# Kernel tuning notes

Hardware: AMD Instinct MI355X
Metric: run time of the kernel (lower is better)

## Reference

```python
import jax, jax.numpy as jnp
import numpy as np

B, S, D = 2, 2048, 1024
H, DK = 16, 64


def setup_inputs() -> dict:
    key = jax.random.key(0)
    ks = jax.random.split(key, 10)
    scale = D ** -0.5
    x = jax.random.normal(ks[0], (B, S, D), dtype=jnp.float32)
    mask = jax.random.randint(ks[1], (B, S), 0, 2) > 0  # True = masked positions
    Wq = jax.random.normal(ks[2], (D, H * DK), dtype=jnp.float32) * scale
    Wk = jax.random.normal(ks[3], (D, H * DK), dtype=jnp.float32) * scale
    Wv = jax.random.normal(ks[4], (D, H * DK), dtype=jnp.float32) * scale
    Wo = jax.random.normal(ks[5], (H * DK, D), dtype=jnp.float32) * scale
    bq = jnp.zeros((H * DK,), jnp.float32)
    bk = jnp.zeros((H * DK,), jnp.float32)
    bv = jnp.zeros((H * DK,), jnp.float32)
    bo = jnp.zeros((D,), jnp.float32)
    return {"x": x, "mask": mask, "Wq": Wq, "bq": bq, "Wk": Wk, "bk": bk,
            "Wv": Wv, "bv": bv, "Wo": Wo, "bo": bo}


def reference(x, mask, Wq, bq, Wk, bk, Wv, bv, Wo, bo):
    b, s, _ = x.shape
    # Linear + activation (dropout is identity at eval)
    q = jax.nn.relu(x @ Wq + bq).reshape(b, s, H, DK)
    k = jax.nn.relu(x @ Wk + bk).reshape(b, s, H, DK)
    v = jax.nn.relu(x @ Wv + bv).reshape(b, s, H, DK)
    # scores: [B, H, Sq, Sk]
    attn = jnp.einsum("bqhd,bkhd->bhqk", q, k) * (DK ** -0.5)
    # NOTE: original uses masked_fill(mask, 1e-9) BEFORE softmax (not -inf)
    attn = jnp.where(mask[:, None, None, :], jnp.float32(1e-9), attn)
    attn = jax.nn.softmax(attn, axis=-1)
    out = jnp.einsum("bhqk,bkhd->bqhd", attn, v).reshape(b, s, H * DK)
    return jax.nn.relu(out @ Wo + bo)
```

## Files before the change

### kernel.cpp

```cpp
#include <hip/hip_runtime.h>
#include <stdint.h>

typedef __attribute__((ext_vector_type(8))) short short8;
typedef __attribute__((ext_vector_type(4))) short short4b;
typedef __attribute__((ext_vector_type(4))) float f32x4;
typedef __attribute__((ext_vector_type(4))) unsigned short ushort4_t;

#define MFMA16(a, b, c) __builtin_amdgcn_mfma_f32_16x16x32_bf16((a), (b), (c), 0, 0, 0)

#if defined(__HIP_DEVICE_COMPILE__)
  #if __has_builtin(__builtin_amdgcn_mfma_f32_16x16x16bf16_1k)
    #define MFMA16K16(a, b, c) __builtin_amdgcn_mfma_f32_16x16x16bf16_1k((a), (b), (c), 0, 0, 0)
  #else
    #define MFMA16K16(a, b, c) __builtin_amdgcn_mfma_f32_16x16x16_bf16((a), (b), (c), 0, 0, 0)
  #endif
#else
  #define MFMA16K16(a, b, c) (c)
#endif

#define SCL_F (0.125f * 1.44269504f)

__device__ __forceinline__ float b2f(unsigned short u) {
    union { unsigned u; float f; } c; c.u = ((unsigned)u) << 16; return c.f;
}
__device__ __forceinline__ unsigned short f2b(float f) {
    union { float f; unsigned u; } c; c.f = f;
    unsigned r = c.u + 0x7FFF + ((c.u >> 16) & 1);
    return (unsigned short)(r >> 16);
}
__device__ __forceinline__ unsigned f_as_u(float f) {
    union { float f; unsigned u; } c; c.f = f; return c.u;
}

__device__ __forceinline__ void g2lds16(const unsigned short* g, unsigned lds_byte_off) {
    __builtin_amdgcn_global_load_lds(
        (const __attribute__((address_space(1))) void*)(uintptr_t)g,
        (__attribute__((address_space(3))) void*)(uintptr_t)lds_byte_off,
        16, 0, 0);
}

__global__ void detect_dtype(const unsigned short* __restrict__ x, int* __restrict__ flag) {
    __shared__ int cnt;
    if (threadIdx.x == 0) cnt = 0;
    __syncthreads();
    int insane = 0;
    #pragma unroll
    for (int j = 0; j < 4; ++j) {
        unsigned short u = x[threadIdx.x * 4 + j];
        int e = (u >> 7) & 0xFF;
        if ((e >= 1 && e <= 90) || e >= 165) insane++;
    }
    atomicAdd(&cnt, insane);
    __syncthreads();
    if (threadIdx.x == 0) *flag = (cnt > 128) ? 1 : 0;
}

__global__ __launch_bounds__(256) void convtrans_k(const void* __restrict__ s0, const void* __restrict__ s1,
                                                   const void* __restrict__ s2, const void* __restrict__ s3,
                                                   const void* __restrict__ b0, const void* __restrict__ b1,
                                                   const void* __restrict__ b2, const void* __restrict__ b3s,
                                                   const void* __restrict__ xsrc,
                                                   unsigned short* __restrict__ xdst,
                                                   unsigned short* __restrict__ dstBase,
                                                   unsigned short* __restrict__ dstB3,
                                                   unsigned short* __restrict__ dstBo,
                                                   const int* __restrict__ flag) {
    const int z = blockIdx.z;
    if (z >= 5) {
        if (!*flag) return;
        const int slice = z - 5;
        const size_t i0 = (size_t)slice * 524288 + (blockIdx.y * 16 + blockIdx.x) * 2048 + threadIdx.x * 8;
        const float* s = (const float*)xsrc;
        float4 f0 = *(const float4*)&s[i0];
        float4 f1 = *(const float4*)&s[i0 + 4];
        unsigned short* t = &xdst[i0];
        t[0] = f2b(f0.x); t[1] = f2b(f0.y); t[2] = f2b(f0.z); t[3] = f2b(f0.w);
        t[4] = f2b(f1.x); t[5] = f2b(f1.y); t[6] = f2b(f1.z); t[7] = f2b(f1.w);
        return;
    }
    if (z == 4) {
        if (blockIdx.y != 0 || blockIdx.x >= 4) return;
        const int w = blockIdx.x;
        const void* src = (w == 0) ? b0 : (w == 1) ? b1 : (w == 2) ? b2 : b3s;
        const float bscl = (w == 0) ? SCL_F : 1.0f;
        #pragma unroll
        for (int j = 0; j < 4; ++j) {
            const int i = threadIdx.x * 4 + j;
            float fv = (*flag) ? ((const float*)src)[i] : b2f(((const unsigned short*)src)[i]);
            unsigned short v = f2b(fv * bscl);
            if (w < 3) dstB3[w * 1024 + i] = v;
            else dstBo[i] = v;
        }
        return;
    }
    __shared__ __align__(16) unsigned short tile[64 * 72];
    const void* src = (z == 0) ? s0 : (z == 1) ? s1 : (z == 2) ? s2 : s3;
    unsigned short* dst = dstBase + (size_t)z * 1024 * 1024;
    const float wscl = (z == 0) ? SCL_F : 1.0f;
    const int tid = threadIdx.x;
    const int r0 = blockIdx.y * 64, c0 = blockIdx.x * 64;
    const int rb = tid >> 3, c = (tid & 7) * 8;
    if (*flag) {
        const float* s = (const float*)src;
        #pragma unroll
        for (int it = 0; it < 2; ++it) {
            int rr = it * 32 + rb;
            float4 f0 = *(const float4*)&s[(size_t)(r0 + rr) * 1024 + c0 + c];
            float4 f1 = *(const float4*)&s[(size_t)(r0 + rr) * 1024 + c0 + c + 4];
            unsigned short* t = &tile[rr * 72 + c];
            t[0] = f2b(f0.x * wscl); t[1] = f2b(f0.y * wscl); t[2] = f2b(f0.z * wscl); t[3] = f2b(f0.w * wscl);
            t[4] = f2b(f1.x * wscl); t[5] = f2b(f1.y * wscl); t[6] = f2b(f1.z * wscl); t[7] = f2b(f1.w * wscl);
        }
    } else if (z == 0) {
        const unsigned short* s = (const unsigned short*)src;
        #pragma unroll
        for (int it = 0; it < 2; ++it) {
            int rr = it * 32 + rb;
            union { short8 v; unsigned short u[8]; } in;
            in.v = *(const short8*)&s[(size_t)(r0 + rr) * 1024 + c0 + c];
            unsigned short* t = &tile[rr * 72 + c];
            #pragma unroll
            for (int j = 0; j < 8; ++j) t[j] = f2b(b2f(in.u[j]) * SCL_F);
        }
    } else {
        const unsigned short* s = (const unsigned short*)src;
        #pragma unroll
        for (int it = 0; it < 2; ++it) {
            int rr = it * 32 + rb;
            *(short8*)&tile[rr * 72 + c] = *(const short8*)&s[(size_t)(r0 + rr) * 1024 + c0 + c];
        }
    }
    __syncthreads();
    #pragma unroll
    for (int it = 0; it < 2; ++it) {
        int n = it * 32 + rb, k8 = c;
        union { short8 s; unsigned short u[8]; } tmp;
        #pragma unroll
        for (int j = 0; j < 8; ++j) tmp.u[j] = tile[(k8 + j) * 72 + n];
        *(short8*)&dst[(size_t)(c0 + n) * 1024 + r0 + k8] = tmp.s;
    }
}

__global__ __launch_bounds__(256) void mask_k(unsigned short* __restrict__ qkv,
                                              const int* __restrict__ mask) {
    const int row = blockIdx.x * 2 + (threadIdx.x >> 7);
    const int col = (threadIdx.x & 127) * 8;
    if (mask[row]) {
        const short8 z = {0, 0, 0, 0, 0, 0, 0, 0};
        *(short8*)&qkv[(size_t)row * 3072 + 1024 + col] = z;
    }
}

__global__ __launch_bounds__(256) void gemm_bias_relu(const unsigned short* __restrict__ A,
                                                      const void* __restrict__ Araw,
                                                      const unsigned short* __restrict__ BT,
                                                      const unsigned short* __restrict__ bias,
                                                      void* __restrict__ C,
                                                      unsigned short* __restrict__ VtG,
                                                      const int* __restrict__ flag,
                                                      int M, int N, int K, int mode) {
    __shared__ __align__(16) unsigned short As[128 * 32];
    __shared__ __align__(16) unsigned short Bs[128 * 32];
    const int tid = threadIdx.x;
    const int wave = tid >> 6, lane = tid & 63;
    const int quad = lane >> 4, l16 = lane & 15;
    const int wm = wave >> 1, wn = wave & 1;
    const int m0 = blockIdx.y * 128, n0 = blockIdx.x * 128;

    const unsigned short* Ause = (Araw != nullptr && *flag == 0) ? (const unsigned short*)Araw : A;

    f32x4 acc[4][4];
    #pragma unroll
    for (int i = 0; i < 4; i++)
        #pragma unroll
        for (int j = 0; j < 4; j++) acc[i][j] = (f32x4){0.f, 0.f, 0.f, 0.f};

    const int srow = wave * 32 + (lane >> 2);
    const int sc8  = (lane & 3) * 8;
    const unsigned short* gA0 = Ause + (size_t)(m0 + srow) * K + sc8;
    const unsigned short* gA1 = gA0 + (size_t)16 * K;
    const unsigned short* gB0 = BT + (size_t)(n0 + srow) * K + sc8;
    const unsigned short* gB1 = gB0 + (size_t)16 * K;
    const unsigned ldsA = (unsigned)(uintptr_t)&As[0] + wave * 2048;
    const unsigned ldsB = (unsigned)(uintptr_t)&Bs[0] + wave * 2048;

    for (int k0 = 0; k0 < K; k0 += 32) {
        __syncthreads();
        g2lds16(gA0 + k0, ldsA);
        g2lds16(gA1 + k0, ldsA + 1024);
        g2lds16(gB0 + k0, ldsB);
        g2lds16(gB1 + k0, ldsB + 1024);
        __syncthreads();
        short8 af[4], bf[4];
        #pragma unroll
        for (int i = 0; i < 4; i++) af[i] = *(const short8*)&As[(wm * 64 + i * 16 + l16) * 32 + quad * 8];
        #pragma unroll
        for (int j = 0; j < 4; j++) bf[j] = *(const short8*)&Bs[(wn * 64 + j * 16 + l16) * 32 + quad * 8];
        #pragma unroll
        for (int i = 0; i < 4; i++)
            #pragma unroll
            for (int j = 0; j < 4; j++)
                acc[i][j] = MFMA16(af[i], bf[j], acc[i][j]);
    }

    if (mode == 2 && n0 >= 2048) {
        #pragma unroll
        for (int j = 0; j < 4; j++) {
            const int col = n0 + wn * 64 + j * 16 + l16;
            const int h  = (col - 2048) >> 6;
            const int dk = (col - 2048) & 63;
            const float bj = b2f(bias[col]);
            #pragma unroll
            for (int i = 0; i < 4; i++) {
                const int rowb = m0 + wm * 64 + i * 16 + quad * 4;
                const int bb = rowb >> 11;
                const int s0 = rowb & 2047;
                ushort4_t w;
                #pragma unroll
                for (int r = 0; r < 4; r++) {
                    float v = acc[i][j][r] + bj;
                    v = v > 0.f ? v : 0.f;
                    w[r] = f2b(v);
                }
                *(ushort4_t*)&VtG[(size_t)((bb * 16 + h) * 64 + dk) * 2048 + s0] = w;
            }
        }
    } else {
        const int f32out = (mode == 1) && (*flag != 0);
        #pragma unroll
        for (int j = 0; j < 4; j++) {
            const int col = n0 + wn * 64 + j * 16 + l16;
            const float bj = b2f(bias[col]);
            #pragma unroll
            for (int i = 0; i < 4; i++) {
                const int rowb = m0 + wm * 64 + i * 16 + quad * 4;
                #pragma unroll
                for (int r = 0; r < 4; r++) {
                    float v = acc[i][j][r] + bj;
                    v = v > 0.f ? v : 0.f;
                    if (f32out) ((float*)C)[(size_t)(rowb + r) * N + col] = v;
                    else ((unsigned short*)C)[(size_t)(rowb + r) * N + col] = f2b(v);
                }
            }
        }
    }
}

__global__ __launch_bounds__(256) void attn_kernel(const unsigned short* __restrict__ qkv,
                                                   const unsigned short* __restrict__ VtG,
                                                   unsigned short* __restrict__ out) {
    __shared__ __align__(16) unsigned short Ks[64 * 72];
    __shared__ __align__(16) unsigned short Vs[64 * 72];

    const int qt = blockIdx.x, bh = blockIdx.y;
    const int b = bh >> 4, h = bh & 15;
    const int tid = threadIdx.x, wave = tid >> 6, lane = tid & 63;
    const int quad = lane >> 4, l16 = lane & 15;

    const int qrowA = qt * 128 + wave * 16 + l16;
    const unsigned short* qpA = qkv + (size_t)(b * 2048 + qrowA) * 3072 + h * 64;
    const unsigned short* qpB = qpA + (size_t)64 * 3072;
    const short8 qa0 = *(const short8*)(qpA + quad * 8);
    const short8 qa1 = *(const short8*)(qpA + 32 + quad * 8);
    const short8 qb0 = *(const short8*)(qpB + quad * 8);
    const short8 qb1 = *(const short8*)(qpB + 32 + quad * 8);

    f32x4 oA[4], oB[4], sumA, sumB;
    #pragma unroll
    for (int n = 0; n < 4; n++) { oA[n] = (f32x4){0.f,0.f,0.f,0.f}; oB[n] = (f32x4){0.f,0.f,0.f,0.f}; }
    sumA = (f32x4){0.f,0.f,0.f,0.f};
    sumB = (f32x4){0.f,0.f,0.f,0.f};

    const short4b ones = { (short)0x3F80, (short)0x3F80, (short)0x3F80, (short)0x3F80 };

    const int srow = tid >> 2;
    const int scol = (tid & 3) * 16;
    const unsigned short* kg = qkv + (size_t)(b * 2048 + srow) * 3072 + 1024 + h * 64 + scol;
    const unsigned short* vg = VtG + (size_t)(bh * 64 + srow) * 2048 + scol;
    const size_t kstep = (size_t)64 * 3072;
    unsigned short* wK = &Ks[srow * 72 + scol];
    unsigned short* wV = &Vs[srow * 72 + scol];

    for (int kt = 0; kt < 32; ++kt) {
        __syncthreads();
        *(short8*)wK       = *(const short8*)(kg + kt * kstep);
        *(short8*)(wK + 8) = *(const short8*)(kg + kt * kstep + 8);
        *(short8*)wV       = *(const short8*)(vg + kt * 64);
        *(short8*)(wV + 8) = *(const short8*)(vg + kt * 64 + 8);
        __syncthreads();

        f32x4 sA[4], sB[4];
        #pragma unroll
        for (int t = 0; t < 4; ++t) {
            const short8 kb0 = *(const short8*)&Ks[(t * 16 + l16) * 72 + quad * 8];
            const short8 kb1 = *(const short8*)&Ks[(t * 16 + l16) * 72 + 32 + quad * 8];
            f32x4 z = (f32x4){0.f, 0.f, 0.f, 0.f};
            sA[t] = MFMA16(kb1, qa1, MFMA16(kb0, qa0, z));
            sB[t] = MFMA16(kb1, qb1, MFMA16(kb0, qb0, z));
        }

        short4b vb[4][4];
        #pragma unroll
        for (int t = 0; t < 4; ++t)
            #pragma unroll
            for (int n = 0; n < 4; ++n)
                vb[t][n] = *(const short4b*)&Vs[(n * 16 + l16) * 72 + t * 16 + quad * 4];

        #pragma unroll
        for (int t = 0; t < 4; ++t) {
            float pA[4], pB[4];
            #pragma unroll
            for (int r = 0; r < 4; ++r) {
                pA[r] = exp2f(sA[t][r]);
                pB[r] = exp2f(sB[t][r]);
            }
            union { unsigned u[2]; short4b s; } fa, fb;
            fa.u[0] = __builtin_amdgcn_perm(f_as_u(pA[1]), f_as_u(pA[0]), 0x07060302u);
            fa.u[1] = __builtin_amdgcn_perm(f_as_u(pA[3]), f_as_u(pA[2]), 0x07060302u);
            fb.u[0] = __builtin_amdgcn_perm(f_as_u(pB[1]), f_as_u(pB[0]), 0x07060302u);
            fb.u[1] = __builtin_amdgcn_perm(f_as_u(pB[3]), f_as_u(pB[2]), 0x07060302u);
            #pragma unroll
            for (int n = 0; n < 4; ++n) {
                oA[n] = MFMA16K16(fa.s, vb[t][n], oA[n]);
                oB[n] = MFMA16K16(fb.s, vb[t][n], oB[n]);
            }
            sumA = MFMA16K16(fa.s, ones, sumA);
            sumB = MFMA16K16(fb.s, ones, sumB);
        }
    }

    float invA[4], invB[4];
    #pragma unroll
    for (int r = 0; r < 4; ++r) { invA[r] = 1.0f / sumA[r]; invB[r] = 1.0f / sumB[r]; }
    #pragma unroll
    for (int n = 0; n < 4; n++)
        #pragma unroll
        for (int r = 0; r < 4; r++) {
            const int row = qt * 128 + wave * 16 + quad * 4 + r;
            out[(size_t)(b * 2048 + row) * 1024 + h * 64 + n * 16 + l16] = f2b(oA[n][r] * invA[r]);
            out[(size_t)(b * 2048 + row + 64) * 1024 + h * 64 + n * 16 + l16] = f2b(oB[n][r] * invB[r]);
        }
}

extern "C" void kernel_launch(void* const* d_in, const int* in_sizes, int n_in,
                              void* d_out, int out_size, void* d_ws, size_t ws_size,
                              hipStream_t stream) {
    const void* x  = d_in[0];
    const int*  mk = (const int*)d_in[1];
    const void* Wq = d_in[2]; const void* bq = d_in[3];
    const void* Wk = d_in[4]; const void* bk = d_in[5];
    const void* Wv = d_in[6]; const void* bv = d_in[7];
    const void* Wo = d_in[8]; const void* bo = d_in[9];

    char* wsb = (char*)d_ws;
    int* flag = (int*)wsb;
    unsigned short* W0 = (unsigned short*)(wsb + 64);

    const size_t M1 = 1024u * 1024u;
    const size_t M4 = 4096u * 1024u;
    unsigned short* xb  = W0;
    unsigned short* WT  = xb + M4;
    unsigned short* WoT = WT + 3 * M1;
    unsigned short* b3  = WoT + M1;
    unsigned short* bob = b3 + 4096;
    unsigned short* qkv = bob + 1024;
    unsigned short* VtG = qkv + (size_t)4096 * 3072;
    unsigned short* abf = xb;

    detect_dtype<<<1, 256, 0, stream>>>((const unsigned short*)x, flag);

    convtrans_k<<<dim3(16, 16, 13), 256, 0, stream>>>(Wq, Wk, Wv, Wo, bq, bk, bv, bo,
                                                      x, xb, WT, b3, bob, flag);

    gemm_bias_relu<<<dim3(24, 32), 256, 0, stream>>>(xb, x, WT, b3, qkv, VtG, flag,
                                                     4096, 3072, 1024, 2);
    mask_k<<<2048, 256, 0, stream>>>(qkv, mk);
    attn_kernel<<<dim3(16, 32), 256, 0, stream>>>(qkv, VtG, abf);
    gemm_bias_relu<<<dim3(8, 32), 256, 0, stream>>>(abf, nullptr, WoT, bob, d_out, VtG, flag,
                                                    4096, 1024, 1024, 1);
}
```

Before: 235.7 us.

## Prefetch next K/V tile into registers, XOR-swizzle LDS, raise MFMA priority

The attention kernel now loads the next K and V tile from global memory into registers while the current tile is being computed. This hides global-load latency behind the MFMA work. The padded 72-wide LDS rows become 64-wide rows with an XOR swizzle on 8-element groups, which avoids bank conflicts and shrinks shared memory. s_setprio raises wave priority around the compute section. The register prefetch costs extra VGPRs, which may reduce occupancy.

```diff
diff --git a/kernel.cpp b/kernel.cpp
--- a/kernel.cpp
+++ b/kernel.cpp
@@ -249,8 +249,8 @@
 __global__ __launch_bounds__(256) void attn_kernel(const unsigned short* __restrict__ qkv,
                                                    const unsigned short* __restrict__ VtG,
                                                    unsigned short* __restrict__ out) {
-    __shared__ __align__(16) unsigned short Ks[64 * 72];
-    __shared__ __align__(16) unsigned short Vs[64 * 72];
+    __shared__ __align__(16) unsigned short Ks[64 * 64];
+    __shared__ __align__(16) unsigned short Vs[64 * 64];
 
     const int qt = blockIdx.x, bh = blockIdx.y;
     const int b = bh >> 4, h = bh & 15;
@@ -275,25 +275,42 @@
 
     const int srow = tid >> 2;
     const int scol = (tid & 3) * 16;
+    const int sxor = (srow & 7) << 3;
     const unsigned short* kg = qkv + (size_t)(b * 2048 + srow) * 3072 + 1024 + h * 64 + scol;
     const unsigned short* vg = VtG + (size_t)(bh * 64 + srow) * 2048 + scol;
     const size_t kstep = (size_t)64 * 3072;
-    unsigned short* wK = &Ks[srow * 72 + scol];
-    unsigned short* wV = &Vs[srow * 72 + scol];
+    unsigned short* wK0 = &Ks[(srow * 64 + scol) ^ sxor];
+    unsigned short* wK1 = &Ks[(srow * 64 + scol + 8) ^ sxor];
+    unsigned short* wV0 = &Vs[(srow * 64 + scol) ^ sxor];
+    unsigned short* wV1 = &Vs[(srow * 64 + scol + 8) ^ sxor];
+
+    const int rx = (l16 & 7) << 3;
+
+    short8 rk0 = *(const short8*)(kg);
+    short8 rk1 = *(const short8*)(kg + 8);
+    short8 rv0 = *(const short8*)(vg);
+    short8 rv1 = *(const short8*)(vg + 8);
 
     for (int kt = 0; kt < 32; ++kt) {
         __syncthreads();
-        *(short8*)wK       = *(const short8*)(kg + kt * kstep);
-        *(short8*)(wK + 8) = *(const short8*)(kg + kt * kstep + 8);
-        *(short8*)wV       = *(const short8*)(vg + kt * 64);
-        *(short8*)(wV + 8) = *(const short8*)(vg + kt * 64 + 8);
+        *(short8*)wK0 = rk0;
+        *(short8*)wK1 = rk1;
+        *(short8*)wV0 = rv0;
+        *(short8*)wV1 = rv1;
+        if (kt < 31) {
+            rk0 = *(const short8*)(kg + (kt + 1) * kstep);
+            rk1 = *(const short8*)(kg + (kt + 1) * kstep + 8);
+            rv0 = *(const short8*)(vg + (kt + 1) * 64);
+            rv1 = *(const short8*)(vg + (kt + 1) * 64 + 8);
+        }
         __syncthreads();
 
+        __builtin_amdgcn_s_setprio(1);
         f32x4 sA[4], sB[4];
         #pragma unroll
         for (int t = 0; t < 4; ++t) {
-            const short8 kb0 = *(const short8*)&Ks[(t * 16 + l16) * 72 + quad * 8];
-            const short8 kb1 = *(const short8*)&Ks[(t * 16 + l16) * 72 + 32 + quad * 8];
+            const short8 kb0 = *(const short8*)&Ks[(((t * 16 + l16) * 64) + quad * 8) ^ rx];
+            const short8 kb1 = *(const short8*)&Ks[(((t * 16 + l16) * 64) + 32 + quad * 8) ^ rx];
             f32x4 z = (f32x4){0.f, 0.f, 0.f, 0.f};
             sA[t] = MFMA16(kb1, qa1, MFMA16(kb0, qa0, z));
             sB[t] = MFMA16(kb1, qb1, MFMA16(kb0, qb0, z));
@@ -304,7 +321,7 @@
         for (int t = 0; t < 4; ++t)
             #pragma unroll
             for (int n = 0; n < 4; ++n)
-                vb[t][n] = *(const short4b*)&Vs[(n * 16 + l16) * 72 + t * 16 + quad * 4];
+                vb[t][n] = *(const short4b*)&Vs[(((n * 16 + l16) * 64) + t * 16 + quad * 4) ^ rx];
 
         #pragma unroll
         for (int t = 0; t < 4; ++t) {
@@ -327,6 +344,7 @@
             sumA = MFMA16K16(fa.s, ones, sumA);
             sumB = MFMA16K16(fb.s, ones, sumB);
         }
+        __builtin_amdgcn_s_setprio(0);
     }
 
     float invA[4], invB[4];
```

Measured after the change: 227.2 us. -3.6%, faster.

## Pipeline GEMM and attention K/V loads with multi-buffered LDS and swizzle

Applied to the files above, without the earlier changes.

The GEMM now uses a three-stage LDS ring filled by async global-to-LDS loads, gated by vmcnt waits, so loads for later K-steps overlap the current MFMAs. The attention kernel double-buffers K/V tiles through registers, swaps padded LDS rows for an XOR swizzle, and remaps block indices for locality. It also raises wave priority during MFMA work and uses the hardware exp2 builtin. The intent is to hide global-load latency and cut barrier stalls, at the cost of more LDS (possibly lower occupancy) and fragile hand-set wait counts.

```diff
diff --git a/kernel.cpp b/kernel.cpp
--- a/kernel.cpp
+++ b/kernel.cpp
@@ -14,8 +14,14 @@
   #else
     #define MFMA16K16(a, b, c) __builtin_amdgcn_mfma_f32_16x16x16_bf16((a), (b), (c), 0, 0, 0)
   #endif
+  #if __has_builtin(__builtin_amdgcn_exp2f)
+    #define EXP2(x) __builtin_amdgcn_exp2f(x)
+  #else
+    #define EXP2(x) exp2f(x)
+  #endif
 #else
   #define MFMA16K16(a, b, c) (c)
+  #define EXP2(x) exp2f(x)
 #endif
 
 #define SCL_F (0.125f * 1.44269504f)
@@ -159,8 +165,8 @@
                                                       unsigned short* __restrict__ VtG,
                                                       const int* __restrict__ flag,
                                                       int M, int N, int K, int mode) {
-    __shared__ __align__(16) unsigned short As[128 * 32];
-    __shared__ __align__(16) unsigned short Bs[128 * 32];
+    __shared__ __align__(16) unsigned short As[3][128 * 32];
+    __shared__ __align__(16) unsigned short Bs[3][128 * 32];
     const int tid = threadIdx.x;
     const int wave = tid >> 6, lane = tid & 63;
     const int quad = lane >> 4, l16 = lane & 15;
@@ -181,26 +187,60 @@
     const unsigned short* gA1 = gA0 + (size_t)16 * K;
     const unsigned short* gB0 = BT + (size_t)(n0 + srow) * K + sc8;
     const unsigned short* gB1 = gB0 + (size_t)16 * K;
-    const unsigned ldsA = (unsigned)(uintptr_t)&As[0] + wave * 2048;
-    const unsigned ldsB = (unsigned)(uintptr_t)&Bs[0] + wave * 2048;
+
+    unsigned lA0 = (unsigned)(uintptr_t)&As[0][0] + wave * 2048;
+    unsigned lA1 = (unsigned)(uintptr_t)&As[1][0] + wave * 2048;
+    unsigned lA2 = (unsigned)(uintptr_t)&As[2][0] + wave * 2048;
+    unsigned lB0 = (unsigned)(uintptr_t)&Bs[0][0] + wave * 2048;
+    unsigned lB1 = (unsigned)(uintptr_t)&Bs[1][0] + wave * 2048;
+    unsigned lB2 = (unsigned)(uintptr_t)&Bs[2][0] + wave * 2048;
+    const unsigned short* pA0 = &As[0][0];
+    const unsigned short* pA1 = &As[1][0];
+    const unsigned short* pA2 = &As[2][0];
+    const unsigned short* pB0 = &Bs[0][0];
+    const unsigned short* pB1 = &Bs[1][0];
+    const unsigned short* pB2 = &Bs[2][0];
+
+    g2lds16(gA0, lA0); g2lds16(gA1, lA0 + 1024);
+    g2lds16(gB0, lB0); g2lds16(gB1, lB0 + 1024);
+    if (32 < K) {
+        g2lds16(gA0 + 32, lA1); g2lds16(gA1 + 32, lA1 + 1024);
+        g2lds16(gB0 + 32, lB1); g2lds16(gB1 + 32, lB1 + 1024);
+    }
+    if (64 < K) {
+        g2lds16(gA0 + 64, lA2); g2lds16(gA1 + 64, lA2 + 1024);
+        g2lds16(gB0 + 64, lB2); g2lds16(gB1 + 64, lB2 + 1024);
+    }
 
     for (int k0 = 0; k0 < K; k0 += 32) {
-        __syncthreads();
-        g2lds16(gA0 + k0, ldsA);
-        g2lds16(gA1 + k0, ldsA + 1024);
-        g2lds16(gB0 + k0, ldsB);
-        g2lds16(gB1 + k0, ldsB + 1024);
-        __syncthreads();
+        if (k0 + 64 < K)       asm volatile("s_waitcnt vmcnt(8)" ::: "memory");
+        else if (k0 + 32 < K)  asm volatile("s_waitcnt vmcnt(4)" ::: "memory");
+        else                   asm volatile("s_waitcnt vmcnt(0)" ::: "memory");
+        __builtin_amdgcn_s_barrier();
+
         short8 af[4], bf[4];
         #pragma unroll
-        for (int i = 0; i < 4; i++) af[i] = *(const short8*)&As[(wm * 64 + i * 16 + l16) * 32 + quad * 8];
-        #pragma unroll
-        for (int j = 0; j < 4; j++) bf[j] = *(const short8*)&Bs[(wn * 64 + j * 16 + l16) * 32 + quad * 8];
+        for (int i = 0; i < 4; i++) af[i] = *(const short8*)&pA0[(wm * 64 + i * 16 + l16) * 32 + quad * 8];
+        #pragma unroll
+        for (int j = 0; j < 4; j++) bf[j] = *(const short8*)&pB0[(wn * 64 + j * 16 + l16) * 32 + quad * 8];
         #pragma unroll
         for (int i = 0; i < 4; i++)
             #pragma unroll
             for (int j = 0; j < 4; j++)
                 acc[i][j] = MFMA16(af[i], bf[j], acc[i][j]);
+
+        __builtin_amdgcn_s_barrier();
+
+        if (k0 + 96 < K) {
+            g2lds16(gA0 + k0 + 96, lA0); g2lds16(gA1 + k0 + 96, lA0 + 1024);
+            g2lds16(gB0 + k0 + 96, lB0); g2lds16(gB1 + k0 + 96, lB0 + 1024);
+        }
+        unsigned tu;
+        tu = lA0; lA0 = lA1; lA1 = lA2; lA2 = tu;
+        tu = lB0; lB0 = lB1; lB1 = lB2; lB2 = tu;
+        const unsigned short* tp;
+        tp = pA0; pA0 = pA1; pA1 = pA2; pA2 = tp;
+        tp = pB0; pB0 = pB1; pB1 = pB2; pB2 = tp;
     }
 
     if (mode == 2 && n0 >= 2048) {
@@ -246,13 +286,57 @@
     }
 }
 
+#define ATTN_TILE(Kbuf, Vbuf)                                                            \
+    do {                                                                                 \
+        __builtin_amdgcn_s_setprio(1);                                                   \
+        f32x4 sA[4], sB[4];                                                              \
+        _Pragma("unroll")                                                                \
+        for (int t = 0; t < 4; ++t) {                                                    \
+            const short8 kb0 = *(const short8*)&(Kbuf)[(((t * 16 + l16) * 64) + quad * 8) ^ rx];       \
+            const short8 kb1 = *(const short8*)&(Kbuf)[(((t * 16 + l16) * 64) + 32 + quad * 8) ^ rx];  \
+            f32x4 z = (f32x4){0.f, 0.f, 0.f, 0.f};                                       \
+            sA[t] = MFMA16(kb1, qa1, MFMA16(kb0, qa0, z));                               \
+            sB[t] = MFMA16(kb1, qb1, MFMA16(kb0, qb0, z));                               \
+        }                                                                                \
+        short4b vb[4][4];                                                                \
+        _Pragma("unroll")                                                                \
+        for (int t = 0; t < 4; ++t)                                                      \
+            _Pragma("unroll")                                                            \
+            for (int n = 0; n < 4; ++n)                                                  \
+                vb[t][n] = *(const short4b*)&(Vbuf)[(((n * 16 + l16) * 64) + t * 16 + quad * 4) ^ rx]; \
+        _Pragma("unroll")                                                                \
+        for (int t = 0; t < 4; ++t) {                                                    \
+            float pA[4], pB[4];                                                          \
+            _Pragma("unroll")                                                            \
+            for (int r = 0; r < 4; ++r) {                                                \
+                pA[r] = EXP2(sA[t][r]);                                                  \
+                pB[r] = EXP2(sB[t][r]);                                                  \
+            }                                                                            \
+            union { unsigned u[2]; short4b s; } fa, fb;                                  \
+            fa.u[0] = __builtin_amdgcn_perm(f_as_u(pA[1]), f_as_u(pA[0]), 0x07060302u);  \
+            fa.u[1] = __builtin_amdgcn_perm(f_as_u(pA[3]), f_as_u(pA[2]), 0x07060302u);  \
+            fb.u[0] = __builtin_amdgcn_perm(f_as_u(pB[1]), f_as_u(pB[0]), 0x07060302u);  \
+            fb.u[1] = __builtin_amdgcn_perm(f_as_u(pB[3]), f_as_u(pB[2]), 0x07060302u);  \
+            _Pragma("unroll")                                                            \
+            for (int n = 0; n < 4; ++n) {                                                \
+                oA[n] = MFMA16K16(fa.s, vb[t][n], oA[n]);                                \
+                oB[n] = MFMA16K16(fb.s, vb[t][n], oB[n]);                                \
+            }                                                                            \
+            sumA = MFMA16K16(fa.s, ones, sumA);                                          \
+            sumB = MFMA16K16(fb.s, ones, sumB);                                          \
+        }                                                                                \
+        __builtin_amdgcn_s_setprio(0);                                                   \
+    } while (0)
+
 __global__ __launch_bounds__(256) void attn_kernel(const unsigned short* __restrict__ qkv,
                                                    const unsigned short* __restrict__ VtG,
                                                    unsigned short* __restrict__ out) {
-    __shared__ __align__(16) unsigned short Ks[64 * 72];
-    __shared__ __align__(16) unsigned short Vs[64 * 72];
-
-    const int qt = blockIdx.x, bh = blockIdx.y;
+    __shared__ __align__(16) unsigned short Ks[2][64 * 64];
+    __shared__ __align__(16) unsigned short Vs[2][64 * 64];
+
+    const int l = blockIdx.y * 16 + blockIdx.x;
+    const int v = (l & 7) * 64 + (l >> 3);
+    const int qt = v & 15, bh = v >> 4;
     const int b = bh >> 4, h = bh & 15;
     const int tid = threadIdx.x, wave = tid >> 6, lane = tid & 63;
     const int quad = lane >> 4, l16 = lane & 15;
@@ -275,58 +359,55 @@
 
     const int srow = tid >> 2;
     const int scol = (tid & 3) * 16;
+    const int sxor = (srow & 7) << 3;
     const unsigned short* kg = qkv + (size_t)(b * 2048 + srow) * 3072 + 1024 + h * 64 + scol;
     const unsigned short* vg = VtG + (size_t)(bh * 64 + srow) * 2048 + scol;
     const size_t kstep = (size_t)64 * 3072;
-    unsigned short* wK = &Ks[srow * 72 + scol];
-    unsigned short* wV = &Vs[srow * 72 + scol];
-
-    for (int kt = 0; kt < 32; ++kt) {
+    const int sidx0 = (srow * 64 + scol) ^ sxor;
+    const int sidx1 = (srow * 64 + scol + 8) ^ sxor;
+    unsigned short* wK0a = &Ks[0][sidx0];  unsigned short* wK1a = &Ks[0][sidx1];
+    unsigned short* wV0a = &Vs[0][sidx0];  unsigned short* wV1a = &Vs[0][sidx1];
+    unsigned short* wK0b = &Ks[1][sidx0];  unsigned short* wK1b = &Ks[1][sidx1];
+    unsigned short* wV0b = &Vs[1][sidx0];  unsigned short* wV1b = &Vs[1][sidx1];
+
+    const int rx = (l16 & 7) << 3;
+
+    short8 rkA0 = *(const short8*)(kg);
+    short8 rkA1 = *(const short8*)(kg + 8);
+    short8 rvA0 = *(const short8*)(vg);
+    short8 rvA1 = *(const short8*)(vg + 8);
+    *(short8*)wK0a = rkA0;  *(short8*)wK1a = rkA1;
+    *(short8*)wV0a = rvA0;  *(short8*)wV1a = rvA1;
+    short8 rkB0 = *(const short8*)(kg + kstep);
+    short8 rkB1 = *(const short8*)(kg + kstep + 8);
+    short8 rvB0 = *(const short8*)(vg + 64);
+    short8 rvB1 = *(const short8*)(vg + 64 + 8);
+    __syncthreads();
+
+    for (int kt = 0; kt < 32; kt += 2) {
+        *(short8*)wK0b = rkB0;  *(short8*)wK1b = rkB1;
+        *(short8*)wV0b = rvB0;  *(short8*)wV1b = rvB1;
+        if (kt + 2 < 32) {
+            rkA0 = *(const short8*)(kg + (kt + 2) * kstep);
+            rkA1 = *(const short8*)(kg + (kt + 2) * kstep + 8);
+            rvA0 = *(const short8*)(vg + (kt + 2) * 64);
+            rvA1 = *(const short8*)(vg + (kt + 2) * 64 + 8);
+        }
+        ATTN_TILE(Ks[0], Vs[0]);
         __syncthreads();
-        *(short8*)wK       = *(const short8*)(kg + kt * kstep);
-        *(short8*)(wK + 8) = *(const short8*)(kg + kt * kstep + 8);
-        *(short8*)wV       = *(const short8*)(vg + kt * 64);
-        *(short8*)(wV + 8) = *(const short8*)(vg + kt * 64 + 8);
+
+        if (kt + 2 < 32) {
+            *(short8*)wK0a = rkA0;  *(short8*)wK1a = rkA1;
+            *(short8*)wV0a = rvA0;  *(short8*)wV1a = rvA1;
+        }
+        if (kt + 3 < 32) {
+            rkB0 = *(const short8*)(kg + (kt + 3) * kstep);
+            rkB1 = *(const short8*)(kg + (kt + 3) * kstep + 8);
+            rvB0 = *(const short8*)(vg + (kt + 3) * 64);
+            rvB1 = *(const short8*)(vg + (kt + 3) * 64 + 8);
+        }
+        ATTN_TILE(Ks[1], Vs[1]);
         __syncthreads();
-
-        f32x4 sA[4], sB[4];
-        #pragma unroll
-        for (int t = 0; t < 4; ++t) {
-            const short8 kb0 = *(const short8*)&Ks[(t * 16 + l16) * 72 + quad * 8];
-            const short8 kb1 = *(const short8*)&Ks[(t * 16 + l16) * 72 + 32 + quad * 8];
-            f32x4 z = (f32x4){0.f, 0.f, 0.f, 0.f};
-            sA[t] = MFMA16(kb1, qa1, MFMA16(kb0, qa0, z));
-            sB[t] = MFMA16(kb1, qb1, MFMA16(kb0, qb0, z));
-        }
-
-        short4b vb[4][4];
-        #pragma unroll
-        for (int t = 0; t < 4; ++t)
-            #pragma unroll
-            for (int n = 0; n < 4; ++n)
-                vb[t][n] = *(const short4b*)&Vs[(n * 16 + l16) * 72 + t * 16 + quad * 4];
-
-        #pragma unroll
-        for (int t = 0; t < 4; ++t) {
-            float pA[4], pB[4];
-            #pragma unroll
-            for (int r = 0; r < 4; ++r) {
-                pA[r] = exp2f(sA[t][r]);
-                pB[r] = exp2f(sB[t][r]);
-            }
-            union { unsigned u[2]; short4b s; } fa, fb;
-            fa.u[0] = __builtin_amdgcn_perm(f_as_u(pA[1]), f_as_u(pA[0]), 0x07060302u);
-            fa.u[1] = __builtin_amdgcn_perm(f_as_u(pA[3]), f_as_u(pA[2]), 0x07060302u);
-            fb.u[0] = __builtin_amdgcn_perm(f_as_u(pB[1]), f_as_u(pB[0]), 0x07060302u);
-            fb.u[1] = __builtin_amdgcn_perm(f_as_u(pB[3]), f_as_u(pB[2]), 0x07060302u);
-            #pragma unroll
-            for (int n = 0; n < 4; ++n) {
-                oA[n] = MFMA16K16(fa.s, vb[t][n], oA[n]);
-                oB[n] = MFMA16K16(fb.s, vb[t][n], oB[n]);
-            }
-            sumA = MFMA16K16(fa.s, ones, sumA);
-            sumB = MFMA16K16(fb.s, ones, sumB);
-        }
     }
 
     float invA[4], invB[4];
```

Result: faster. 197.2 us (-16.4%).
